# Kernel tuning notes

Hardware: AMD Instinct MI355X
Metric: run time of the kernel (lower is better)

The kernel has to match this reference:

```python
import jax, jax.numpy as jnp
import numpy as np

H = 16  # num_heads

def setup_inputs() -> dict:
    key = jax.random.key(0)
    ks = jax.random.split(key, 5)
    B, L, D = 2, 2048, 1024
    x = jax.random.normal(ks[0], (B, L, D), dtype=jnp.float32)
    # causal mask: masked_fill where mask == 0
    attn_mask = jnp.tril(jnp.ones((L, L), dtype=jnp.int32))
    scale = 1.0 / np.sqrt(D)
    Wq = jax.random.normal(ks[1], (D, D), dtype=jnp.float32) * scale
    Wk = jax.random.normal(ks[2], (D, D), dtype=jnp.float32) * scale
    Wv = jax.random.normal(ks[3], (D, D), dtype=jnp.float32) * scale
    Wo = jax.random.normal(ks[4], (D, D), dtype=jnp.float32) * scale
    return {"x": x, "attn_mask": attn_mask, "Wq": Wq, "Wk": Wk, "Wv": Wv, "Wo": Wo}

def reference(x, attn_mask, Wq, Wk, Wv, Wo):
    B, L, D = x.shape
    dh = D // H
    # nn.Linear with no bias: y = x @ W^T
    q = (x @ Wq.T).reshape(B, L, H, dh)
    k = (x @ Wk.T).reshape(B, L, H, dh)
    v = (x @ Wv.T).reshape(B, L, H, dh)
    # scores: [B, H, L, L]
    scores = jnp.einsum('blhd,bmhd->bhlm', q, k) / jnp.sqrt(jnp.array(dh, x.dtype))
    scores = jnp.where(attn_mask == 0, -jnp.inf, scores)
    attn = jax.nn.softmax(scores, axis=-1)
    out = jnp.einsum('bhlm,bmhd->blhd', attn, v).reshape(B, L, D)
    return out @ Wo.T
```

## Files before the change

kernel.cpp:

```cpp
#include <hip/hip_runtime.h>
#include <math.h>

#define L_SEQ  2048
#define D_MODEL 1024
#define N_HEAD 16
#define D_HEAD 64
#define B_SIZE 2

typedef __attribute__((ext_vector_type(8))) short bf16x8;
typedef __attribute__((ext_vector_type(4))) float f32x4;
typedef unsigned short u16;
typedef unsigned int u32;

__device__ __forceinline__ f32x4 mfma16(bf16x8 a, bf16x8 b, f32x4 c) {
    return __builtin_amdgcn_mfma_f32_16x16x32_bf16(a, b, c, 0, 0, 0);
}

__device__ __forceinline__ u16 f2bf(float x) {
    u32 u = __builtin_bit_cast(u32, x);
    u32 r = (u + 0x7FFFu + ((u >> 16) & 1u)) >> 16;
    return (u16)r;
}
__device__ __forceinline__ u16 f2bf_t(float x) {
    return (u16)(__builtin_bit_cast(u32, x) >> 16);
}
__device__ __forceinline__ float bf2f(u16 h) {
    u32 u = ((u32)h) << 16;
    return __builtin_bit_cast(float, u);
}

__device__ __forceinline__ void gl2lds16(const void* g, void* l) {
    __builtin_amdgcn_global_load_lds(
        (__attribute__((address_space(1))) void*)(g),
        (__attribute__((address_space(3))) void*)(l), 16, 0, 0);
}

__global__ __launch_bounds__(256) void split_all(
    const float* __restrict__ x,
    const float* __restrict__ w0, const float* __restrict__ w1,
    const float* __restrict__ w2, const float* __restrict__ w3,
    u16* __restrict__ x2, u16* __restrict__ wout) {
    const int id = blockIdx.x;
    const float* in;
    u16* out;
    int idx;
    if (id < 4096) {
        in = x; out = x2; idx = id * 256 + threadIdx.x;
    } else {
        const int wi = (id - 4096) >> 10;
        const int blk = (id - 4096) & 1023;
        in = (wi == 0) ? w0 : (wi == 1) ? w1 : (wi == 2) ? w2 : w3;
        out = wout + (size_t)wi * 2097152;
        idx = blk * 256 + threadIdx.x;
    }
    const int c4 = idx << 2;
    const int r = c4 >> 10, c = c4 & 1023;
    float4 v = *(const float4*)(in + c4);
    u16 h0 = f2bf(v.x), h1 = f2bf(v.y), h2 = f2bf(v.z), h3 = f2bf(v.w);
    ushort4 hi = make_ushort4(h0, h1, h2, h3);
    ushort4 lo = make_ushort4(f2bf(v.x - bf2f(h0)), f2bf(v.y - bf2f(h1)),
                              f2bf(v.z - bf2f(h2)), f2bf(v.w - bf2f(h3)));
    *(ushort4*)(out + (size_t)r * 2048 + c) = hi;
    *(ushort4*)(out + (size_t)r * 2048 + 1024 + c) = lo;
}

__device__ __forceinline__ int kaOf(int x) {
    return (((x >> 4) == 1) ? 1024 : 0) + ((x << 6) & 1023);
}
__device__ __forceinline__ int kwOf(int x) {
    return (((x >> 4) == 0) ? 1024 : 0) + ((x << 6) & 1023);
}

#define SBAR()  do { __builtin_amdgcn_sched_barrier(0); \
                     __builtin_amdgcn_s_barrier(); \
                     __builtin_amdgcn_sched_barrier(0); } while (0)

__global__ __launch_bounds__(512) void gemm256_qkv(
    const u16* __restrict__ A2, const u16* __restrict__ Wall,
    u16* __restrict__ Qh, u16* __restrict__ Ql,
    u16* __restrict__ Kh, u16* __restrict__ Kl,
    u16* __restrict__ Vh) {
    extern __shared__ __align__(16) u16 smem[];

    const int t = threadIdx.x, l = t & 63, wid = t >> 6;
    const int id = blockIdx.x;
    const int wg = (id & 7) * 32 + (id >> 3);
    const int mt = wg >> 4, ntile = wg & 15;
    const int m0 = mt << 8, n0 = ntile * 192;

    const int wrH = wid >> 2;
    const int wcN = (wid & 3) * 48;

    f32x4 acc[8][3];
#pragma unroll
    for (int i = 0; i < 8; ++i)
#pragma unroll
        for (int j = 0; j < 3; ++j) acc[i][j] = (f32x4){0.f, 0.f, 0.f, 0.f};

    const int sr = t >> 3, sc = t & 7;

    auto stageA = [&](int x, int half) {
        const int koff = kaOf(x);
        u16* dst = smem + (x & 1) * 16384 + half * 8192;
        const u16* srcb = A2 + (size_t)(m0 + half * 128) * 2048 + koff;
#pragma unroll
        for (int p = 0; p < 2; ++p) {
            const int r = sr + p * 64;
            const int ck = sc ^ (r & 7);
            gl2lds16(srcb + (size_t)r * 2048 + ck * 8, dst + t * 8 + p * 4096);
        }
    };
    auto stageB = [&](int x, int third) {
        const int koff = kwOf(x);
        u16* dst = smem + 32768 + (x & 1) * 12288 + third * 4096;
        const int r = sr;
        const int ck = sc ^ (r & 7);
        const u16* src = Wall + (size_t)(n0 + third * 64 + r) * 2048 + koff + ck * 8;
        gl2lds16(src, dst + t * 8);
    };
    auto dsA = [&](int s, int mh, int kc, bf16x8 af[4]) {
        const u16* Ab = smem + s * 16384 + wrH * 8192;
#pragma unroll
        for (int f = 0; f < 4; ++f) {
            const int r = mh * 64 + f * 16 + (l & 15);
            const int c8 = kc * 4 + (l >> 4);
            af[f] = *(const bf16x8*)&Ab[r * 64 + ((c8 ^ (r & 7)) << 3)];
        }
    };
    auto dsB = [&](int s, int kc, bf16x8 bfr[3]) {
        const u16* Bb = smem + 32768 + s * 12288;
#pragma unroll
        for (int f = 0; f < 3; ++f) {
            const int row = wcN + f * 16 + (l & 15);
            const int third = row >> 6, lr = row & 63;
            const int c8 = kc * 4 + (l >> 4);
            bfr[f] = *(const bf16x8*)&Bb[third * 4096 + lr * 64 + ((c8 ^ (lr & 7)) << 3)];
        }
    };

    stageB(0, 0); stageB(0, 1); stageB(0, 2);
    stageA(0, 0); stageA(0, 1);
    stageB(1, 0); stageB(1, 1); stageB(1, 2);
    __builtin_amdgcn_sched_barrier(0);
    asm volatile("s_waitcnt vmcnt(3)" ::: "memory");
    __builtin_amdgcn_s_barrier();
    __builtin_amdgcn_sched_barrier(0);

    const int NT = 48;
    bf16x8 breg0[3], breg1[3], af[4];
    for (int tt = 0; tt < NT; ++tt) {
        const int s = tt & 1;
        dsA(s, 0, 0, af); dsB(s, 0, breg0);
        if (tt + 1 < NT) stageA(tt + 1, 0);
        SBAR();
        __builtin_amdgcn_s_setprio(1);
#pragma unroll
        for (int f = 0; f < 4; ++f)
#pragma unroll
            for (int fn = 0; fn < 3; ++fn)
                acc[f][fn] = mfma16(af[f], breg0[fn], acc[f][fn]);
        __builtin_amdgcn_s_setprio(0);
        SBAR();
        dsA(s, 0, 1, af); dsB(s, 1, breg1);
        if (tt + 1 < NT) stageA(tt + 1, 1);
        SBAR();
        __builtin_amdgcn_s_setprio(1);
#pragma unroll
        for (int f = 0; f < 4; ++f)
#pragma unroll
            for (int fn = 0; fn < 3; ++fn)
                acc[f][fn] = mfma16(af[f], breg1[fn], acc[f][fn]);
        __builtin_amdgcn_s_setprio(0);
        SBAR();
        dsA(s, 1, 0, af);
        if (tt + 2 < NT) { stageB(tt + 2, 0); stageB(tt + 2, 1); }
        SBAR();
        __builtin_amdgcn_s_setprio(1);
#pragma unroll
        for (int f = 0; f < 4; ++f)
#pragma unroll
            for (int fn = 0; fn < 3; ++fn)
                acc[4 + f][fn] = mfma16(af[f], breg0[fn], acc[4 + f][fn]);
        __builtin_amdgcn_s_setprio(0);
        SBAR();
        dsA(s, 1, 1, af);
        if (tt + 2 < NT) stageB(tt + 2, 2);
        SBAR();
        __builtin_amdgcn_s_setprio(1);
#pragma unroll
        for (int f = 0; f < 4; ++f)
#pragma unroll
            for (int fn = 0; fn < 3; ++fn)
                acc[4 + f][fn] = mfma16(af[f], breg1[fn], acc[4 + f][fn]);
        __builtin_amdgcn_s_setprio(0);
        __builtin_amdgcn_sched_barrier(0);
        if (tt + 2 < NT) {
            asm volatile("s_waitcnt vmcnt(3)" ::: "memory");
        } else if (tt + 1 < NT) {
            asm volatile("s_waitcnt vmcnt(0)" ::: "memory");
        }
        __builtin_amdgcn_s_barrier();
        __builtin_amdgcn_sched_barrier(0);
    }

#pragma unroll
    for (int fm = 0; fm < 8; ++fm)
#pragma unroll
        for (int fn = 0; fn < 3; ++fn)
#pragma unroll
            for (int rg = 0; rg < 4; ++rg) {
                const int gm = m0 + wrH * 128 + fm * 16 + ((l >> 4) << 2) + rg;
                const int gn = n0 + wcN + fn * 16 + (l & 15);
                const int z = gn >> 10, col = gn & 1023;
                float v = acc[fm][fn][rg];
                if (z == 0) v *= 0.125f;
                const int b = gm >> 11, lq = gm & 2047;
                const int h = col >> 6, d = col & 63;
                const size_t oi = (((size_t)(b * 16 + h)) * 2048 + lq) * 64 + d;
                const u16 hi = f2bf(v);
                if (z == 0) { Qh[oi] = hi; Ql[oi] = f2bf(v - bf2f(hi)); }
                else if (z == 1) { Kh[oi] = hi; Kl[oi] = f2bf(v - bf2f(hi)); }
                else { Vh[oi] = hi; }
            }
}

__global__ __launch_bounds__(256) void gemm_wo(
    const u16* __restrict__ A2, const u16* __restrict__ W2,
    float* __restrict__ Cout) {
    __shared__ __align__(16) u16 As[128 * 32];
    __shared__ __align__(16) u16 Ws2[64 * 32];
    const int t = threadIdx.x, l = t & 63, wid = t >> 6;
    const int id = blockIdx.x;
    const int nid = ((id & 7) << 6) + (id >> 3);
    const int m0 = (nid >> 4) << 7;
    const int n0 = (nid & 15) << 6;
    const int wm = wid >> 1, wn = wid & 1;

    f32x4 acc[4][2];
#pragma unroll
    for (int i = 0; i < 4; ++i)
#pragma unroll
        for (int j = 0; j < 2; ++j) acc[i][j] = (f32x4){0.f, 0.f, 0.f, 0.f};

    const int arow0 = t >> 2, ach0 = (t & 3) ^ (arow0 & 3);
    const int arow1 = (t + 256) >> 2, ach1 = (t & 3) ^ (arow1 & 3);
    const int brow = t >> 2, bch = (t & 3) ^ (brow & 3);

    for (int k0 = 0; k0 < 3072; k0 += 32) {
        const int rg3 = k0 >> 10, kb = k0 & 1023;
        const int ka = (rg3 == 1 ? 1024 : 0) + kb;
        const int kw = (rg3 == 0 ? 1024 : 0) + kb;
        __syncthreads();
        gl2lds16(A2 + (size_t)(m0 + arow0) * 2048 + ka + ach0 * 8,
                 (u16*)As + t * 8);
        gl2lds16(A2 + (size_t)(m0 + arow1) * 2048 + ka + ach1 * 8,
                 (u16*)As + (t + 256) * 8);
        if (t < 256)
            gl2lds16(W2 + (size_t)(n0 + brow) * 2048 + kw + bch * 8,
                     (u16*)Ws2 + t * 8);
        __syncthreads();
        bf16x8 af[4], bfr[2];
#pragma unroll
        for (int f = 0; f < 4; ++f) {
            const int row = wm * 64 + f * 16 + (l & 15);
            const int ch = (l >> 4) ^ (row & 3);
            af[f] = *(const bf16x8*)&As[(row << 5) + (ch << 3)];
        }
#pragma unroll
        for (int f = 0; f < 2; ++f) {
            const int rown = wn * 32 + f * 16 + (l & 15);
            const int chn = (l >> 4) ^ (rown & 3);
            bfr[f] = *(const bf16x8*)&Ws2[(rown << 5) + (chn << 3)];
        }
        __builtin_amdgcn_s_setprio(1);
#pragma unroll
        for (int fm = 0; fm < 4; ++fm)
#pragma unroll
            for (int fn = 0; fn < 2; ++fn)
                acc[fm][fn] = mfma16(af[fm], bfr[fn], acc[fm][fn]);
        __builtin_amdgcn_s_setprio(0);
    }

#pragma unroll
    for (int fm = 0; fm < 4; ++fm)
#pragma unroll
        for (int fn = 0; fn < 2; ++fn)
#pragma unroll
            for (int rg = 0; rg < 4; ++rg) {
                const int gm = m0 + wm * 64 + fm * 16 + ((l >> 4) << 2) + rg;
                const int gn = n0 + wn * 32 + fn * 16 + (l & 15);
                Cout[(size_t)gm * 1024 + gn] = acc[fm][fn][rg];
            }
}

__global__ __launch_bounds__(128) void vtrans(const u16* __restrict__ Vh,
                                              u16* __restrict__ Vth) {
    const int t = threadIdx.x;
    const int kt = (blockIdx.x << 1) + (t >> 6);
    const int h = blockIdx.y, b = blockIdx.z;
    const size_t base = ((size_t)(b * 16 + h)) * 131072;
    const int kv0 = kt << 6;
    const int st = t & 63;
    const int r0 = (st >> 3) << 3;
    const int c0 = (st & 7) << 3;
    ushort4 inv[8][2];
#pragma unroll
    for (int j = 0; j < 8; ++j) {
        const u16* p = Vh + base + (size_t)(kv0 + r0 + j) * 64 + c0;
        inv[j][0] = *(const ushort4*)p;
        inv[j][1] = *(const ushort4*)(p + 4);
    }
#pragma unroll
    for (int i = 0; i < 8; ++i) {
        u16 o[8];
#pragma unroll
        for (int j = 0; j < 8; ++j) {
            ushort4 vv = inv[j][i >> 2];
            const int ii = i & 3;
            o[j] = (ii == 0) ? vv.x : (ii == 1) ? vv.y : (ii == 2) ? vv.z : vv.w;
        }
        u16* q = Vth + base + (size_t)(c0 + i) * 2048 + kv0 + r0;
        *(ushort4*)q = make_ushort4(o[0], o[1], o[2], o[3]);
        *(ushort4*)(q + 4) = make_ushort4(o[4], o[5], o[6], o[7]);
    }
}

struct QTileState {
    bf16x8 qhf[2], qlf[2];
    f32x4 oacc[4];
    float mrow[4], lrow[4];
};

__device__ __forceinline__ void qstate_init(
    QTileState& st, const u16* Qh, const u16* Ql, size_t hb, int q0, int w, int l) {
    const int rowq = q0 + (w << 4) + (l & 15);
#pragma unroll
    for (int kc = 0; kc < 2; ++kc) {
        const size_t off = hb + (size_t)rowq * 64 + (((kc << 2) + (l >> 4)) << 3);
        st.qhf[kc] = *(const bf16x8*)(Qh + off);
        st.qlf[kc] = *(const bf16x8*)(Ql + off);
    }
#pragma unroll
    for (int i = 0; i < 4; ++i) {
        st.oacc[i] = (f32x4){0.f, 0.f, 0.f, 0.f};
        st.mrow[i] = -INFINITY;
        st.lrow[i] = 0.f;
    }
}

__device__ __forceinline__ void fa_qk_softmax(
    QTileState& st, const u16* bKh, const u16* bKl,
    int kv0, int q0, int w, int l, u16 pb[4][4]) {
    f32x4 sacc[4];
#pragma unroll
    for (int nf = 0; nf < 4; ++nf) sacc[nf] = (f32x4){0.f, 0.f, 0.f, 0.f};
#pragma unroll
    for (int kc = 0; kc < 2; ++kc) {
        bf16x8 kh_[4], kl_[4];
#pragma unroll
        for (int nf = 0; nf < 4; ++nf) {
            const int row = (nf << 4) + (l & 15);
            const int ch = ((kc << 2) + (l >> 4)) ^ (row & 7);
            kh_[nf] = *(const bf16x8*)&bKh[(row << 6) + (ch << 3)];
            kl_[nf] = *(const bf16x8*)&bKl[(row << 6) + (ch << 3)];
        }
        __builtin_amdgcn_s_setprio(1);
#pragma unroll
        for (int nf = 0; nf < 4; ++nf) {
            sacc[nf] = mfma16(st.qhf[kc], kl_[nf], sacc[nf]);
            sacc[nf] = mfma16(st.qlf[kc], kh_[nf], sacc[nf]);
            sacc[nf] = mfma16(st.qhf[kc], kh_[nf], sacc[nf]);
        }
        __builtin_amdgcn_s_setprio(0);
    }

    const bool domask = (kv0 + 63) > (q0 + (w << 4));
    float pm[4] = {-INFINITY, -INFINITY, -INFINITY, -INFINITY};
    float sv[4][4];
#pragma unroll
    for (int nf = 0; nf < 4; ++nf)
#pragma unroll
        for (int rg = 0; rg < 4; ++rg) {
            float x = sacc[nf][rg];
            if (domask) {
                const int colg = kv0 + (nf << 4) + (l & 15);
                const int rowg = q0 + (w << 4) + ((l >> 4) << 2) + rg;
                if (colg > rowg) x = -INFINITY;
            }
            sv[nf][rg] = x;
            pm[rg] = fmaxf(pm[rg], x);
        }
#pragma unroll
    for (int rg = 0; rg < 4; ++rg) {
        float v = pm[rg];
        v = fmaxf(v, __shfl_xor(v, 1));
        v = fmaxf(v, __shfl_xor(v, 2));
        v = fmaxf(v, __shfl_xor(v, 4));
        v = fmaxf(v, __shfl_xor(v, 8));
        pm[rg] = v;
    }
    const float need = fmaxf(fmaxf(pm[0] - st.mrow[0], pm[1] - st.mrow[1]),
                             fmaxf(pm[2] - st.mrow[2], pm[3] - st.mrow[3]));
    if (__any(need > 8.0f)) {
#pragma unroll
        for (int rg = 0; rg < 4; ++rg) {
            const float mn = fmaxf(st.mrow[rg], pm[rg]);
            const float al = __expf(st.mrow[rg] - mn);
            st.mrow[rg] = mn;
            st.lrow[rg] *= al;
#pragma unroll
            for (int nf = 0; nf < 4; ++nf) st.oacc[nf][rg] *= al;
        }
    }
    float ps[4] = {0.f, 0.f, 0.f, 0.f};
#pragma unroll
    for (int nf = 0; nf < 4; ++nf)
#pragma unroll
        for (int rg = 0; rg < 4; ++rg) {
            const float p = __expf(sv[nf][rg] - st.mrow[rg]);
            ps[rg] += p;
            pb[nf][rg] = f2bf_t(p);
        }
#pragma unroll
    for (int rg = 0; rg < 4; ++rg) {
        float v = ps[rg];
        v += __shfl_xor(v, 1);
        v += __shfl_xor(v, 2);
        v += __shfl_xor(v, 4);
        v += __shfl_xor(v, 8);
        st.lrow[rg] += v;
    }
}

__device__ __forceinline__ void fa_writeP(const u16 pb[4][4], int l, u16* Pw) {
#pragma unroll
    for (int nf = 0; nf < 4; ++nf)
#pragma unroll
        for (int rg = 0; rg < 4; ++rg) {
            const int r = ((l >> 4) << 2) + rg;
            const int c = (nf << 4) + (l & 15);
            const int ch = (c >> 3) ^ (r & 7);
            Pw[(r << 6) + (ch << 3) + (c & 7)] = pb[nf][rg];
        }
}

__device__ __forceinline__ void fa_epilogue(
    QTileState& st, u16* A2, int g, int q0, int w, int l) {
    const int b = g >> 4, h = g & 15;
    float inv[4];
#pragma unroll
    for (int rg = 0; rg < 4; ++rg) inv[rg] = 1.0f / st.lrow[rg];
#pragma unroll
    for (int nf = 0; nf < 4; ++nf)
#pragma unroll
        for (int rg = 0; rg < 4; ++rg) {
            const int rowq = q0 + (w << 4) + ((l >> 4) << 2) + rg;
            const int m = (b << 11) + rowq;
            const int d = (nf << 4) + (l & 15);
            const float v = st.oacc[nf][rg] * inv[rg];
            const u16 hi = f2bf(v);
            const u16 lo = f2bf(v - bf2f(hi));
            const size_t rb = (size_t)m * 2048;
            A2[rb + h * 64 + d] = hi;
            A2[rb + 1024 + h * 64 + d] = lo;
        }
}

__global__ __launch_bounds__(512) void flash_mfma(
    const u16* __restrict__ Qh, const u16* __restrict__ Ql,
    const u16* __restrict__ Kh, const u16* __restrict__ Kl,
    const u16* __restrict__ Vth,
    u16* __restrict__ A2) {
    extern __shared__ __align__(16) u16 smem[];
    u16* const KhsA = smem;
    u16* const KlsA = smem + 4096;
    u16* const VhsA = smem + 8192;
    u16* const KhsB = smem + 12288;
    u16* const KlsB = smem + 16384;
    u16* const VhsB = smem + 20480;
    u16* const PsB  = smem + 24576;
    u16* const PsA  = smem + 32768;

    const int t = threadIdx.x, l = t & 63, w = t >> 6;
    const int id = blockIdx.x;
    const int nid = ((id & 7) << 5) + (id >> 3);
    const int g = nid >> 3;
    const int p = nid & 7;
    const int q0A = p << 7;
    const int q0B = (15 - p) << 7;
    const size_t hb = (size_t)g * 131072;

    QTileState stA, stB;
    qstate_init(stA, Qh, Ql, hb, q0A, w, l);
    qstate_init(stB, Qh, Ql, hb, q0B, w, l);

    const int row_s = t >> 3;
    const int cs_s = (t & 7) ^ (row_s & 7);

    auto stage = [&](u16* dKh, u16* dKl, u16* dVh, int kt_) {
        const int kv0s = kt_ << 6;
        const size_t koff = hb + (size_t)(kv0s + row_s) * 64 + cs_s * 8;
        gl2lds16(Kh + koff, dKh + t * 8);
        gl2lds16(Kl + koff, dKl + t * 8);
        const size_t voff = hb + (size_t)row_s * 2048 + kv0s + cs_s * 8;
        gl2lds16(Vth + voff, dVh + t * 8);
    };

    u16* const PwB = PsB + (w << 10);
    u16* const PwA = PsA + (w << 10);
    const int ntA = (p << 1) + 2;
    const int ntB = 32 - (p << 1);

    auto unit = [&](const u16* bKh, const u16* bKl, const u16* bVh, int kt_) {
        const int kv0 = kt_ << 6;
        const bool aB = kv0 <= q0B + (w << 4) + 15;
        const bool aA = (kt_ < ntA) && (kv0 <= q0A + (w << 4) + 15);
        if (!aB && !aA) return;
        u16 pbB[4][4], pbA[4][4];
        if (aB) fa_qk_softmax(stB, bKh, bKl, kv0, q0B, w, l, pbB);
        if (aA) fa_qk_softmax(stA, bKh, bKl, kv0, q0A, w, l, pbA);
        if (aB) fa_writeP(pbB, l, PwB);
        if (aA) fa_writeP(pbA, l, PwA);
#pragma unroll
        for (int kc = 0; kc < 2; ++kc) {
            bf16x8 vh_[4];
#pragma unroll
            for (int nf = 0; nf < 4; ++nf) {
                const int row = (nf << 4) + (l & 15);
                const int cv = ((kc << 2) + (l >> 4)) ^ (row & 7);
                vh_[nf] = *(const bf16x8*)&bVh[(row << 6) + (cv << 3)];
            }
            const int r = l & 15;
            const int chp = ((kc << 2) + (l >> 4)) ^ (r & 7);
            __builtin_amdgcn_s_setprio(1);
            if (aB) {
                const bf16x8 pa = *(const bf16x8*)&PwB[(r << 6) + (chp << 3)];
#pragma unroll
                for (int nf = 0; nf < 4; ++nf)
                    stB.oacc[nf] = mfma16(pa, vh_[nf], stB.oacc[nf]);
            }
            if (aA) {
                const bf16x8 pa = *(const bf16x8*)&PwA[(r << 6) + (chp << 3)];
#pragma unroll
                for (int nf = 0; nf < 4; ++nf)
                    stA.oacc[nf] = mfma16(pa, vh_[nf], stA.oacc[nf]);
            }
            __builtin_amdgcn_s_setprio(0);
        }
    };

    stage(KhsA, KlsA, VhsA, 0);
    __syncthreads();
    for (int kt = 0; kt < ntB; kt += 2) {
        stage(KhsB, KlsB, VhsB, kt + 1);
        unit(KhsA, KlsA, VhsA, kt);
        __syncthreads();
        if (kt + 2 < ntB) stage(KhsA, KlsA, VhsA, kt + 2);
        unit(KhsB, KlsB, VhsB, kt + 1);
        __syncthreads();
    }

    fa_epilogue(stA, A2, g, q0A, w, l);
    fa_epilogue(stB, A2, g, q0B, w, l);
}

__global__ __launch_bounds__(256) void gemm_bt_f32(
    const float* __restrict__ A, const float* __restrict__ W,
    float* __restrict__ C, int M, int N, int K) {
    __shared__ float As[16][68];
    __shared__ float Bs[16][68];
    const int t = threadIdx.x;
    const int tx = t & 15, ty = t >> 4;
    const int m0 = blockIdx.y << 6, n0 = blockIdx.x << 6;
    const int lr = t >> 2, lc = (t & 3) << 2;
    const float* Ag = A + (size_t)(m0 + lr) * K + lc;
    const float* Wg = W + (size_t)(n0 + lr) * K + lc;
    float acc[4][4];
#pragma unroll
    for (int i = 0; i < 4; ++i)
#pragma unroll
        for (int j = 0; j < 4; ++j) acc[i][j] = 0.f;
    for (int k0 = 0; k0 < K; k0 += 16) {
        const float4 av = *(const float4*)(Ag + k0);
        const float4 wv = *(const float4*)(Wg + k0);
        __syncthreads();
        As[lc + 0][lr] = av.x; As[lc + 1][lr] = av.y;
        As[lc + 2][lr] = av.z; As[lc + 3][lr] = av.w;
        Bs[lc + 0][lr] = wv.x; Bs[lc + 1][lr] = wv.y;
        Bs[lc + 2][lr] = wv.z; Bs[lc + 3][lr] = wv.w;
        __syncthreads();
#pragma unroll
        for (int kk = 0; kk < 16; ++kk) {
            const float4 a = *(const float4*)&As[kk][ty << 2];
            const float4 b = *(const float4*)&Bs[kk][tx << 2];
            acc[0][0] += a.x * b.x; acc[0][1] += a.x * b.y; acc[0][2] += a.x * b.z; acc[0][3] += a.x * b.w;
            acc[1][0] += a.y * b.x; acc[1][1] += a.y * b.y; acc[1][2] += a.y * b.z; acc[1][3] += a.y * b.w;
            acc[2][0] += a.z * b.x; acc[2][1] += a.z * b.y; acc[2][2] += a.z * b.z; acc[2][3] += a.z * b.w;
            acc[3][0] += a.w * b.x; acc[3][1] += a.w * b.y; acc[3][2] += a.w * b.z; acc[3][3] += a.w * b.w;
        }
    }
#pragma unroll
    for (int i = 0; i < 4; ++i) {
        float4 o;
        o.x = acc[i][0]; o.y = acc[i][1]; o.z = acc[i][2]; o.w = acc[i][3];
        *(float4*)&C[(size_t)(m0 + (ty << 2) + i) * N + n0 + (tx << 2)] = o;
    }
}

#define SW(row, seg) ((((seg) ^ (((row) + ((row) >> 4)) & 15)) << 2))

__global__ __launch_bounds__(256) void flash_f32(
    const float* __restrict__ Q, const float* __restrict__ K,
    const float* __restrict__ V, float* __restrict__ O) {
    __shared__ float Qs[64 * 64];
    __shared__ float KPs[64 * 64];
    __shared__ float Vs[64 * 64];
    const int t = threadIdx.x;
    const int tx = t & 15, ty = t >> 4;
    const int qt = blockIdx.x, h = blockIdx.y, b = blockIdx.z;
    const int q0 = qt << 6;
    const size_t hbase = (size_t)b * L_SEQ * D_MODEL + (size_t)h * D_HEAD;
#pragma unroll
    for (int i = 0; i < 4; ++i) {
        const int idx = t + (i << 8);
        const int rr = idx >> 4, seg = idx & 15;
        const float4 qv = *(const float4*)&Q[hbase + (size_t)(q0 + rr) * D_MODEL + (seg << 2)];
        *(float4*)&Qs[rr * 64 + SW(rr, seg)] = qv;
    }
    float m[4], lr_[4], oacc[4][4];
#pragma unroll
    for (int i = 0; i < 4; ++i) {
        m[i] = -INFINITY; lr_[i] = 0.f;
#pragma unroll
        for (int j = 0; j < 4; ++j) oacc[i][j] = 0.f;
    }
    const int ntile = qt + 1;
    for (int kt = 0; kt < ntile; ++kt) {
        const int kv0 = kt << 6;
        __syncthreads();
#pragma unroll
        for (int i = 0; i < 4; ++i) {
            const int idx = t + (i << 8);
            const int rr = idx >> 4, seg = idx & 15;
            const float4 kv = *(const float4*)&K[hbase + (size_t)(kv0 + rr) * D_MODEL + (seg << 2)];
            const float4 vv = *(const float4*)&V[hbase + (size_t)(kv0 + rr) * D_MODEL + (seg << 2)];
            *(float4*)&KPs[rr * 64 + SW(rr, seg)] = kv;
            *(float4*)&Vs[rr * 64 + SW(rr, seg)] = vv;
        }
        __syncthreads();
        float s[4][4];
#pragma unroll
        for (int i = 0; i < 4; ++i)
#pragma unroll
            for (int j = 0; j < 4; ++j) s[i][j] = 0.f;
#pragma unroll
        for (int seg = 0; seg < 16; ++seg) {
            float4 qv[4], kv[4];
#pragma unroll
            for (int i = 0; i < 4; ++i) {
                const int R = (ty << 2) + i;
                qv[i] = *(const float4*)&Qs[R * 64 + SW(R, seg)];
            }
#pragma unroll
            for (int j = 0; j < 4; ++j) {
                const int Cc = (tx << 2) + j;
                kv[j] = *(const float4*)&KPs[Cc * 64 + SW(Cc, seg)];
            }
#pragma unroll
            for (int i = 0; i < 4; ++i)
#pragma unroll
                for (int j = 0; j < 4; ++j)
                    s[i][j] += qv[i].x * kv[j].x + qv[i].y * kv[j].y +
                               qv[i].z * kv[j].z + qv[i].w * kv[j].w;
        }
        const bool diag = (kt == qt);
        float tm[4];
#pragma unroll
        for (int i = 0; i < 4; ++i) {
            tm[i] = -INFINITY;
#pragma unroll
            for (int j = 0; j < 4; ++j) {
                float sval = s[i][j] * 0.125f;
                if (diag) {
                    const int Cg = kv0 + (tx << 2) + j;
                    const int Rg = q0 + (ty << 2) + i;
                    if (Cg > Rg) sval = -INFINITY;
                }
                s[i][j] = sval;
                tm[i] = fmaxf(tm[i], sval);
            }
            tm[i] = fmaxf(tm[i], __shfl_xor(tm[i], 1));
            tm[i] = fmaxf(tm[i], __shfl_xor(tm[i], 2));
            tm[i] = fmaxf(tm[i], __shfl_xor(tm[i], 4));
            tm[i] = fmaxf(tm[i], __shfl_xor(tm[i], 8));
        }
        float p[4][4];
#pragma unroll
        for (int i = 0; i < 4; ++i) {
            const float mn = fmaxf(m[i], tm[i]);
            const float alpha = __expf(m[i] - mn);
            m[i] = mn;
            float psum = 0.f;
#pragma unroll
            for (int j = 0; j < 4; ++j) {
                p[i][j] = __expf(s[i][j] - mn);
                psum += p[i][j];
            }
            psum += __shfl_xor(psum, 1);
            psum += __shfl_xor(psum, 2);
            psum += __shfl_xor(psum, 4);
            psum += __shfl_xor(psum, 8);
            lr_[i] = lr_[i] * alpha + psum;
#pragma unroll
            for (int j = 0; j < 4; ++j) oacc[i][j] *= alpha;
        }
        __syncthreads();
#pragma unroll
        for (int i = 0; i < 4; ++i) {
            const int R = (ty << 2) + i;
            float4 pv;
            pv.x = p[i][0]; pv.y = p[i][1]; pv.z = p[i][2]; pv.w = p[i][3];
            *(float4*)&KPs[R * 64 + SW(R, tx)] = pv;
        }
        __syncthreads();
#pragma unroll
        for (int cs = 0; cs < 16; ++cs) {
            float pc[4][4];
            float4 vr[4];
#pragma unroll
            for (int i = 0; i < 4; ++i) {
                const int R = (ty << 2) + i;
                const float4 pr = *(const float4*)&KPs[R * 64 + SW(R, cs)];
                pc[i][0] = pr.x; pc[i][1] = pr.y; pc[i][2] = pr.z; pc[i][3] = pr.w;
            }
#pragma unroll
            for (int cc = 0; cc < 4; ++cc) {
                const int Cr = (cs << 2) + cc;
                vr[cc] = *(const float4*)&Vs[Cr * 64 + SW(Cr, tx)];
            }
#pragma unroll
            for (int i = 0; i < 4; ++i)
#pragma unroll
                for (int cc = 0; cc < 4; ++cc) {
                    oacc[i][0] += pc[i][cc] * vr[cc].x;
                    oacc[i][1] += pc[i][cc] * vr[cc].y;
                    oacc[i][2] += pc[i][cc] * vr[cc].z;
                    oacc[i][3] += pc[i][cc] * vr[cc].w;
                }
        }
    }
#pragma unroll
    for (int i = 0; i < 4; ++i) {
        const int R = (ty << 2) + i;
        const float invl = 1.0f / lr_[i];
        float4 o;
        o.x = oacc[i][0] * invl; o.y = oacc[i][1] * invl;
        o.z = oacc[i][2] * invl; o.w = oacc[i][3] * invl;
        *(float4*)&O[hbase + (size_t)(q0 + R) * D_MODEL + (tx << 2)] = o;
    }
}

extern "C" void kernel_launch(void* const* d_in, const int* in_sizes, int n_in,
                              void* d_out, int out_size, void* d_ws, size_t ws_size,
                              hipStream_t stream) {
    const float* x  = (const float*)d_in[0];
    const float* Wq = (const float*)d_in[2];
    const float* Wk = (const float*)d_in[3];
    const float* Wv = (const float*)d_in[4];
    const float* Wo = (const float*)d_in[5];
    float* out = (float*)d_out;

    if (ws_size >= 83886080ull) {
        char* ws = (char*)d_ws;
        u16* x2  = (u16*)(ws);
        u16* Wq2 = (u16*)(ws + 16777216);
        u16* Wo2 = (u16*)(ws + 29360128);
        u16* Qh  = (u16*)(ws + 33554432);
        u16* Ql  = (u16*)(ws + 41943040);
        u16* Kh  = (u16*)(ws + 50331648);
        u16* Kl  = (u16*)(ws + 58720256);
        u16* Vth = (u16*)(ws + 67108864);
        u16* Vh  = (u16*)d_out;

        hipFuncSetAttribute((const void*)flash_mfma,
                            hipFuncAttributeMaxDynamicSharedMemorySize, 81920);
        hipFuncSetAttribute((const void*)gemm256_qkv,
                            hipFuncAttributeMaxDynamicSharedMemorySize, 114688);

        split_all<<<8192, 256, 0, stream>>>(x, Wq, Wk, Wv, Wo, x2, Wq2);
        gemm256_qkv<<<256, 512, 114688, stream>>>(x2, Wq2, Qh, Ql, Kh, Kl, Vh);
        vtrans<<<dim3(16, 16, 2), 128, 0, stream>>>(Vh, Vth);
        flash_mfma<<<256, 512, 81920, stream>>>(Qh, Ql, Kh, Kl, Vth, x2);
        gemm_wo<<<512, 256, 0, stream>>>(x2, Wo2, out);
    } else {
        const int M = B_SIZE * L_SEQ, N = D_MODEL, Kd = D_MODEL;
        float* Qw = (float*)d_ws;
        float* Kw = Qw + (size_t)M * D_MODEL;
        float* Vw = Kw + (size_t)M * D_MODEL;
        float* Aw = Vw + (size_t)M * D_MODEL;
        dim3 gg(N / 64, M / 64);
        gemm_bt_f32<<<gg, 256, 0, stream>>>(x, Wq, Qw, M, N, Kd);
        gemm_bt_f32<<<gg, 256, 0, stream>>>(x, Wk, Kw, M, N, Kd);
        gemm_bt_f32<<<gg, 256, 0, stream>>>(x, Wv, Vw, M, N, Kd);
        flash_f32<<<dim3(L_SEQ / 64, N_HEAD, B_SIZE), 256, 0, stream>>>(Qw, Kw, Vw, Aw);
        gemm_bt_f32<<<gg, 256, 0, stream>>>(Aw, Wo, out, M, N, Kd);
    }
}
```

Baseline: 231.8 us.

## Use exp2 softmax, MFMA row sums, and two-tile double-buffered KV staging

Folds log2(e) into the Q scale so softmax can use the raw v_exp_f32 (exp2) instruction, and raises the rescale threshold to match the base-2 domain. Row sums of P are now computed by an extra MFMA against a ones vector instead of a shuffle reduction, which removes cross-lane reduction work from the softmax critical path. KV staging is restructured to load two 64-key tiles per stage into a double buffer, so there is one barrier per pair of tiles instead of one per tile. This raises dynamic LDS to 128 KB, and row sums are now accumulated from bf16-truncated P rather than the fp32 probabilities.

```diff
diff --git a/kernel.cpp b/kernel.cpp
--- a/kernel.cpp
+++ b/kernel.cpp
@@ -27,6 +27,11 @@
 __device__ __forceinline__ float bf2f(u16 h) {
     u32 u = ((u32)h) << 16;
     return __builtin_bit_cast(float, u);
+}
+__device__ __forceinline__ float fexp2(float x) {
+    float r;
+    asm("v_exp_f32 %0, %1" : "=v"(r) : "v"(x));
+    return r;
 }
 
 __device__ __forceinline__ void gl2lds16(const void* g, void* l) {
@@ -213,7 +218,7 @@
                 const int gn = n0 + wcN + fn * 16 + (l & 15);
                 const int z = gn >> 10, col = gn & 1023;
                 float v = acc[fm][fn][rg];
-                if (z == 0) v *= 0.125f;
+                if (z == 0) v *= 0.18033688f;
                 const int b = gm >> 11, lq = gm & 2047;
                 const int h = col >> 6, d = col & 63;
                 const size_t oi = (((size_t)(b * 16 + h)) * 2048 + lq) * 64 + d;
@@ -401,35 +406,22 @@
     }
     const float need = fmaxf(fmaxf(pm[0] - st.mrow[0], pm[1] - st.mrow[1]),
                              fmaxf(pm[2] - st.mrow[2], pm[3] - st.mrow[3]));
-    if (__any(need > 8.0f)) {
+    if (__any(need > 11.5f)) {
 #pragma unroll
         for (int rg = 0; rg < 4; ++rg) {
             const float mn = fmaxf(st.mrow[rg], pm[rg]);
-            const float al = __expf(st.mrow[rg] - mn);
+            const float al = fexp2(st.mrow[rg] - mn);
             st.mrow[rg] = mn;
             st.lrow[rg] *= al;
 #pragma unroll
             for (int nf = 0; nf < 4; ++nf) st.oacc[nf][rg] *= al;
         }
     }
-    float ps[4] = {0.f, 0.f, 0.f, 0.f};
 #pragma unroll
     for (int nf = 0; nf < 4; ++nf)
 #pragma unroll
-        for (int rg = 0; rg < 4; ++rg) {
-            const float p = __expf(sv[nf][rg] - st.mrow[rg]);
-            ps[rg] += p;
-            pb[nf][rg] = f2bf_t(p);
-        }
-#pragma unroll
-    for (int rg = 0; rg < 4; ++rg) {
-        float v = ps[rg];
-        v += __shfl_xor(v, 1);
-        v += __shfl_xor(v, 2);
-        v += __shfl_xor(v, 4);
-        v += __shfl_xor(v, 8);
-        st.lrow[rg] += v;
-    }
+        for (int rg = 0; rg < 4; ++rg)
+            pb[nf][rg] = f2bf_t(fexp2(sv[nf][rg] - st.mrow[rg]));
 }
 
 __device__ __forceinline__ void fa_writeP(const u16 pb[4][4], int l, u16* Pw) {
@@ -472,14 +464,8 @@
     const u16* __restrict__ Vth,
     u16* __restrict__ A2) {
     extern __shared__ __align__(16) u16 smem[];
-    u16* const KhsA = smem;
-    u16* const KlsA = smem + 4096;
-    u16* const VhsA = smem + 8192;
-    u16* const KhsB = smem + 12288;
-    u16* const KlsB = smem + 16384;
-    u16* const VhsB = smem + 20480;
-    u16* const PsB  = smem + 24576;
-    u16* const PsA  = smem + 32768;
+    u16* const PsB = smem + 49152;
+    u16* const PsA = smem + 57344;
 
     const int t = threadIdx.x, l = t & 63, w = t >> 6;
     const int id = blockIdx.x;
@@ -497,21 +483,29 @@
     const int row_s = t >> 3;
     const int cs_s = (t & 7) ^ (row_s & 7);
 
-    auto stage = [&](u16* dKh, u16* dKl, u16* dVh, int kt_) {
+    auto stage1 = [&](int s, int slot, int kt_) {
+        u16* base = smem + s * 24576 + slot * 12288;
         const int kv0s = kt_ << 6;
         const size_t koff = hb + (size_t)(kv0s + row_s) * 64 + cs_s * 8;
-        gl2lds16(Kh + koff, dKh + t * 8);
-        gl2lds16(Kl + koff, dKl + t * 8);
+        gl2lds16(Kh + koff, base + t * 8);
+        gl2lds16(Kl + koff, base + 4096 + t * 8);
         const size_t voff = hb + (size_t)row_s * 2048 + kv0s + cs_s * 8;
-        gl2lds16(Vth + voff, dVh + t * 8);
+        gl2lds16(Vth + voff, base + 8192 + t * 8);
     };
 
     u16* const PwB = PsB + (w << 10);
     u16* const PwA = PsA + (w << 10);
     const int ntA = (p << 1) + 2;
     const int ntB = 32 - (p << 1);
-
-    auto unit = [&](const u16* bKh, const u16* bKl, const u16* bVh, int kt_) {
+    const int NB = ntB >> 1;
+
+    const short ob = (short)0x3F80;
+    const bf16x8 ones = {ob, ob, ob, ob, ob, ob, ob, ob};
+
+    auto unit = [&](int s, int slot, int kt_) {
+        const u16* bKh = smem + s * 24576 + slot * 12288;
+        const u16* bKl = bKh + 4096;
+        const u16* bVh = bKh + 8192;
         const int kv0 = kt_ << 6;
         const bool aB = kv0 <= q0B + (w << 4) + 15;
         const bool aA = (kt_ < ntA) && (kv0 <= q0A + (w << 4) + 15);
@@ -521,6 +515,7 @@
         if (aA) fa_qk_softmax(stA, bKh, bKl, kv0, q0A, w, l, pbA);
         if (aB) fa_writeP(pbB, l, PwB);
         if (aA) fa_writeP(pbA, l, PwA);
+        f32x4 lsB = {0.f, 0.f, 0.f, 0.f}, lsA = {0.f, 0.f, 0.f, 0.f};
 #pragma unroll
         for (int kc = 0; kc < 2; ++kc) {
             bf16x8 vh_[4];
@@ -538,25 +533,34 @@
 #pragma unroll
                 for (int nf = 0; nf < 4; ++nf)
                     stB.oacc[nf] = mfma16(pa, vh_[nf], stB.oacc[nf]);
+                lsB = mfma16(pa, ones, lsB);
             }
             if (aA) {
                 const bf16x8 pa = *(const bf16x8*)&PwA[(r << 6) + (chp << 3)];
 #pragma unroll
                 for (int nf = 0; nf < 4; ++nf)
                     stA.oacc[nf] = mfma16(pa, vh_[nf], stA.oacc[nf]);
+                lsA = mfma16(pa, ones, lsA);
             }
             __builtin_amdgcn_s_setprio(0);
         }
+        if (aB) {
+#pragma unroll
+            for (int rg = 0; rg < 4; ++rg) stB.lrow[rg] += lsB[rg];
+        }
+        if (aA) {
+#pragma unroll
+            for (int rg = 0; rg < 4; ++rg) stA.lrow[rg] += lsA[rg];
+        }
     };
 
-    stage(KhsA, KlsA, VhsA, 0);
+    stage1(0, 0, 0); stage1(0, 1, 1);
     __syncthreads();
-    for (int kt = 0; kt < ntB; kt += 2) {
-        stage(KhsB, KlsB, VhsB, kt + 1);
-        unit(KhsA, KlsA, VhsA, kt);
-        __syncthreads();
-        if (kt + 2 < ntB) stage(KhsA, KlsA, VhsA, kt + 2);
-        unit(KhsB, KlsB, VhsB, kt + 1);
+    for (int j = 0; j < NB; ++j) {
+        const int s = j & 1;
+        if (j + 1 < NB) { stage1(s ^ 1, 0, 2 * j + 2); stage1(s ^ 1, 1, 2 * j + 3); }
+        unit(s, 0, 2 * j);
+        unit(s, 1, 2 * j + 1);
         __syncthreads();
     }
 
@@ -783,14 +787,14 @@
         u16* Vh  = (u16*)d_out;
 
         hipFuncSetAttribute((const void*)flash_mfma,
-                            hipFuncAttributeMaxDynamicSharedMemorySize, 81920);
+                            hipFuncAttributeMaxDynamicSharedMemorySize, 131072);
         hipFuncSetAttribute((const void*)gemm256_qkv,
                             hipFuncAttributeMaxDynamicSharedMemorySize, 114688);
 
         split_all<<<8192, 256, 0, stream>>>(x, Wq, Wk, Wv, Wo, x2, Wq2);
         gemm256_qkv<<<256, 512, 114688, stream>>>(x2, Wq2, Qh, Ql, Kh, Kl, Vh);
         vtrans<<<dim3(16, 16, 2), 128, 0, stream>>>(Vh, Vth);
-        flash_mfma<<<256, 512, 81920, stream>>>(Qh, Ql, Kh, Kl, Vth, x2);
+        flash_mfma<<<256, 512, 131072, stream>>>(Qh, Ql, Kh, Kl, Vth, x2);
         gemm_wo<<<512, 256, 0, stream>>>(x2, Wo2, out);
     } else {
         const int M = B_SIZE * L_SEQ, N = D_MODEL, Kd = D_MODEL;
```

After: 222.4 us. 4.1% less time.
